# Kernel optimization log

Measured on AMD Instinct MI355X. Metric: run time of the kernel, lower is better.

Reference implementation:

```python
import jax, jax.numpy as jnp
import numpy as np

KERNEL_SIZE = 2  # matches init kernel_size
EPS = 1e-6


def setup_inputs() -> dict:
    key = jax.random.key(0)
    x = jax.random.uniform(key, (8, 64, 256, 256), dtype=jnp.float32)
    return {"x": x}


def reference(x) -> jnp.ndarray:
    k = KERNEL_SIZE
    b, c, h, w = x.shape
    hp, wp = h - k + 1, w - k + 1  # stride-1 unfold output dims
    n = k * k
    # Gather the k*k shifted views (equivalent to unfold(2,k,1).unfold(3,k,1)).
    # Fixed small loop over k*k offsets, not over data dims.
    windows = jnp.stack(
        [x[:, :, i:i + hp, j:j + wp] for i in range(k) for j in range(k)],
        axis=-1,
    )  # (b, c, hp, wp, n)
    windows = windows.reshape(b, c, hp * wp, n)
    p = windows / (jnp.sum(windows, axis=-1, keepdims=True) + EPS)
    ent = -jnp.sum(p * jnp.log(p + EPS), axis=-1)  # (b, c, hp*wp)
    return ent
```

## Files before the change

kernel.cpp:

```cpp
#include <hip/hip_runtime.h>

#define H    256
#define W    256
#define HP   255
#define WP   255
#define PIX  (HP * WP)
#define NBC  512
#define EPS  1e-6f
#define LN2  0.69314718055994531f

#define TPI   8192
#define NBLK  (NBC * TPI / 256)

typedef float f4 __attribute__((ext_vector_type(4)));

__device__ __forceinline__ float wlog(float w) {
    return w * __builtin_amdgcn_logf(w + EPS);
}

__device__ __forceinline__ float ent4(float Wm, float Tm) {
    const float s = Wm + EPS;
    return LN2 * (Wm * __builtin_amdgcn_logf(s) - Tm) * __builtin_amdgcn_rcpf(s);
}

__global__ __launch_bounds__(256) void entropy_k2_kernel(
    const float* __restrict__ x, float* __restrict__ out)
{
    const int t  = blockIdx.x * 256 + threadIdx.x;
    const int bc = t >> 13;
    const int r  = t & (TPI - 1);
    const int q  = r >> 6;
    const int j0 = (r & 63) << 2;
    const int i0 = q << 1;

    const float* img = x + (size_t)bc * (H * W);
    const float* r0p = img + i0 * W + j0;
    const float* r1p = r0p + W;
    const float* r2p = (q == 127) ? r1p : r1p + W;
    const int j4 = (j0 + 4 < W) ? 4 : 3;

    const f4    va = *(const f4*)r0p;
    const f4    vb = *(const f4*)r1p;
    const f4    vc = *(const f4*)r2p;
    const float a4 = r0p[j4];
    const float b4 = r1p[j4];
    const float c4 = r2p[j4];

    const float la0 = wlog(va.x), la1 = wlog(va.y), la2 = wlog(va.z),
                la3 = wlog(va.w), la4 = wlog(a4);
    const float lb0 = wlog(vb.x), lb1 = wlog(vb.y), lb2 = wlog(vb.z),
                lb3 = wlog(vb.w), lb4 = wlog(b4);
    const float lc0 = wlog(vc.x), lc1 = wlog(vc.y), lc2 = wlog(vc.z),
                lc3 = wlog(vc.w), lc4 = wlog(c4);

    const float hwa0 = va.x + va.y, hwa1 = va.y + va.z, hwa2 = va.z + va.w, hwa3 = va.w + a4;
    const float hwb0 = vb.x + vb.y, hwb1 = vb.y + vb.z, hwb2 = vb.z + vb.w, hwb3 = vb.w + b4;
    const float hwc0 = vc.x + vc.y, hwc1 = vc.y + vc.z, hwc2 = vc.z + vc.w, hwc3 = vc.w + c4;
    const float hta0 = la0 + la1, hta1 = la1 + la2, hta2 = la2 + la3, hta3 = la3 + la4;
    const float htb0 = lb0 + lb1, htb1 = lb1 + lb2, htb2 = lb2 + lb3, htb3 = lb3 + lb4;
    const float htc0 = lc0 + lc1, htc1 = lc1 + lc2, htc2 = lc2 + lc3, htc3 = lc3 + lc4;

    f4 e0, e1;
    e0.x = ent4(hwa0 + hwb0, hta0 + htb0);
    e0.y = ent4(hwa1 + hwb1, hta1 + htb1);
    e0.z = ent4(hwa2 + hwb2, hta2 + htb2);
    e0.w = ent4(hwa3 + hwb3, hta3 + htb3);
    e1.x = ent4(hwb0 + hwc0, htb0 + htc0);
    e1.y = ent4(hwb1 + hwc1, htb1 + htc1);
    e1.z = ent4(hwb2 + hwc2, htb2 + htc2);
    e1.w = ent4(hwb3 + hwc3, htb3 + htc3);

    float* o0 = out + (size_t)bc * PIX + i0 * WP + j0;
    float* o1 = o0 + WP;
    const bool full = (j0 != 252);
    const bool row2 = (q != 127);

    if (full) {
        __builtin_nontemporal_store(e0.x, o0 + 0);
        __builtin_nontemporal_store(e0.y, o0 + 1);
        __builtin_nontemporal_store(e0.z, o0 + 2);
        __builtin_nontemporal_store(e0.w, o0 + 3);
        if (row2) {
            __builtin_nontemporal_store(e1.x, o1 + 0);
            __builtin_nontemporal_store(e1.y, o1 + 1);
            __builtin_nontemporal_store(e1.z, o1 + 2);
            __builtin_nontemporal_store(e1.w, o1 + 3);
        }
    } else {
        __builtin_nontemporal_store(e0.x, o0 + 0);
        __builtin_nontemporal_store(e0.y, o0 + 1);
        __builtin_nontemporal_store(e0.z, o0 + 2);
        if (row2) {
            __builtin_nontemporal_store(e1.x, o1 + 0);
            __builtin_nontemporal_store(e1.y, o1 + 1);
            __builtin_nontemporal_store(e1.z, o1 + 2);
        }
    }
}

extern "C" void kernel_launch(void* const* d_in, const int* in_sizes, int n_in,
                              void* d_out, int out_size, void* d_ws, size_t ws_size,
                              hipStream_t stream)
{
    const float* x   = (const float*)d_in[0];
    float*       out = (float*)d_out;
    entropy_k2_kernel<<<dim3(NBLK), 256, 0, stream>>>(x, out);
}
```

Baseline: 227.2 us.

## Process 16-row strips per thread with rolling row reuse of logs

Each thread now walks a 16-row strip, carrying the previous row's horizontal sums of values and w*log(w) terms forward so each input row is loaded and its logs computed once instead of roughly 1.5 times. Grid size shrinks eightfold and launch bounds request 8 blocks per CU. This cuts redundant loads and transcendental work, but it serializes rows within a thread, lowers the number of independent memory requests in flight, and may hurt latency hiding for a bandwidth-bound kernel.

Result: slower. 269.5 us (+18.7%).

```diff
diff --git a/kernel.cpp b/kernel.cpp
--- a/kernel.cpp
+++ b/kernel.cpp
@@ -9,7 +9,9 @@
 #define EPS  1e-6f
 #define LN2  0.69314718055994531f
 
-#define TPI   8192
+#define RPT   16
+#define NRG   16
+#define TPI   (64 * NRG)
 #define NBLK  (NBC * TPI / 256)
 
 typedef float f4 __attribute__((ext_vector_type(4)));
@@ -23,77 +25,62 @@
     return LN2 * (Wm * __builtin_amdgcn_logf(s) - Tm) * __builtin_amdgcn_rcpf(s);
 }
 
-__global__ __launch_bounds__(256) void entropy_k2_kernel(
+__global__ __launch_bounds__(256, 8) void entropy_k2_kernel(
     const float* __restrict__ x, float* __restrict__ out)
 {
     const int t  = blockIdx.x * 256 + threadIdx.x;
-    const int bc = t >> 13;
+    const int bc = t >> 10;
     const int r  = t & (TPI - 1);
-    const int q  = r >> 6;
+    const int rg = r >> 6;
     const int j0 = (r & 63) << 2;
-    const int i0 = q << 1;
+    const int i0 = rg << 4;
+    const int nrows = (rg == NRG - 1) ? (HP - i0) : RPT;
 
-    const float* img = x + (size_t)bc * (H * W);
-    const float* r0p = img + i0 * W + j0;
-    const float* r1p = r0p + W;
-    const float* r2p = (q == 127) ? r1p : r1p + W;
-    const int j4 = (j0 + 4 < W) ? 4 : 3;
+    const int  j4   = (j0 + 4 < W) ? 4 : 3;
+    const bool full = (j0 != 252);
 
-    const f4    va = *(const f4*)r0p;
-    const f4    vb = *(const f4*)r1p;
-    const f4    vc = *(const f4*)r2p;
-    const float a4 = r0p[j4];
-    const float b4 = r1p[j4];
-    const float c4 = r2p[j4];
+    const float* p = x + (size_t)bc * (H * W) + i0 * W + j0;
+    float*       o = out + (size_t)bc * PIX + i0 * WP + j0;
 
-    const float la0 = wlog(va.x), la1 = wlog(va.y), la2 = wlog(va.z),
-                la3 = wlog(va.w), la4 = wlog(a4);
-    const float lb0 = wlog(vb.x), lb1 = wlog(vb.y), lb2 = wlog(vb.z),
-                lb3 = wlog(vb.w), lb4 = wlog(b4);
-    const float lc0 = wlog(vc.x), lc1 = wlog(vc.y), lc2 = wlog(vc.z),
-                lc3 = wlog(vc.w), lc4 = wlog(c4);
+    {
+        const f4    v  = *(const f4*)p;
+        const float v5 = p[j4];
+        const float l0 = wlog(v.x), l1 = wlog(v.y), l2 = wlog(v.z),
+                    l3 = wlog(v.w), l4 = wlog(v5);
+        float hw0 = v.x + v.y, hw1 = v.y + v.z, hw2 = v.z + v.w, hw3 = v.w + v5;
+        float ht0 = l0 + l1,   ht1 = l1 + l2,   ht2 = l2 + l3,   ht3 = l3 + l4;
 
-    const float hwa0 = va.x + va.y, hwa1 = va.y + va.z, hwa2 = va.z + va.w, hwa3 = va.w + a4;
-    const float hwb0 = vb.x + vb.y, hwb1 = vb.y + vb.z, hwb2 = vb.z + vb.w, hwb3 = vb.w + b4;
-    const float hwc0 = vc.x + vc.y, hwc1 = vc.y + vc.z, hwc2 = vc.z + vc.w, hwc3 = vc.w + c4;
-    const float hta0 = la0 + la1, hta1 = la1 + la2, hta2 = la2 + la3, hta3 = la3 + la4;
-    const float htb0 = lb0 + lb1, htb1 = lb1 + lb2, htb2 = lb2 + lb3, htb3 = lb3 + lb4;
-    const float htc0 = lc0 + lc1, htc1 = lc1 + lc2, htc2 = lc2 + lc3, htc3 = lc3 + lc4;
+        p += W;
+        f4    w  = *(const f4*)p;
+        float w5 = p[j4];
 
-    f4 e0, e1;
-    e0.x = ent4(hwa0 + hwb0, hta0 + htb0);
-    e0.y = ent4(hwa1 + hwb1, hta1 + htb1);
-    e0.z = ent4(hwa2 + hwb2, hta2 + htb2);
-    e0.w = ent4(hwa3 + hwb3, hta3 + htb3);
-    e1.x = ent4(hwb0 + hwc0, htb0 + htc0);
-    e1.y = ent4(hwb1 + hwc1, htb1 + htc1);
-    e1.z = ent4(hwb2 + hwc2, htb2 + htc2);
-    e1.w = ent4(hwb3 + hwc3, htb3 + htc3);
+        for (int ii = 0; ii < nrows; ++ii) {
+            const float* pn = (ii + 1 < nrows) ? p + W : p;
+            const f4    n  = *(const f4*)pn;
+            const float n5 = pn[j4];
 
-    float* o0 = out + (size_t)bc * PIX + i0 * WP + j0;
-    float* o1 = o0 + WP;
-    const bool full = (j0 != 252);
-    const bool row2 = (q != 127);
+            const float m0 = wlog(w.x), m1 = wlog(w.y), m2 = wlog(w.z),
+                        m3 = wlog(w.w), m4 = wlog(w5);
+            const float gw0 = w.x + w.y, gw1 = w.y + w.z,
+                        gw2 = w.z + w.w, gw3 = w.w + w5;
+            const float gt0 = m0 + m1, gt1 = m1 + m2,
+                        gt2 = m2 + m3, gt3 = m3 + m4;
 
-    if (full) {
-        __builtin_nontemporal_store(e0.x, o0 + 0);
-        __builtin_nontemporal_store(e0.y, o0 + 1);
-        __builtin_nontemporal_store(e0.z, o0 + 2);
-        __builtin_nontemporal_store(e0.w, o0 + 3);
-        if (row2) {
-            __builtin_nontemporal_store(e1.x, o1 + 0);
-            __builtin_nontemporal_store(e1.y, o1 + 1);
-            __builtin_nontemporal_store(e1.z, o1 + 2);
-            __builtin_nontemporal_store(e1.w, o1 + 3);
-        }
-    } else {
-        __builtin_nontemporal_store(e0.x, o0 + 0);
-        __builtin_nontemporal_store(e0.y, o0 + 1);
-        __builtin_nontemporal_store(e0.z, o0 + 2);
-        if (row2) {
-            __builtin_nontemporal_store(e1.x, o1 + 0);
-            __builtin_nontemporal_store(e1.y, o1 + 1);
-            __builtin_nontemporal_store(e1.z, o1 + 2);
+            const float e0 = ent4(hw0 + gw0, ht0 + gt0);
+            const float e1 = ent4(hw1 + gw1, ht1 + gt1);
+            const float e2 = ent4(hw2 + gw2, ht2 + gt2);
+            const float e3 = ent4(hw3 + gw3, ht3 + gt3);
+
+            __builtin_nontemporal_store(e0, o + 0);
+            __builtin_nontemporal_store(e1, o + 1);
+            __builtin_nontemporal_store(e2, o + 2);
+            if (full)
+                __builtin_nontemporal_store(e3, o + 3);
+
+            hw0 = gw0; hw1 = gw1; hw2 = gw2; hw3 = gw3;
+            ht0 = gt0; ht1 = gt1; ht2 = gt2; ht3 = gt3;
+            w = n; w5 = n5; p = pn;
+            o += WP;
         }
     }
 }
```
